# Optimization experiments

Measured on AMD Instinct MI355X. Metric: run time of the kernel, lower is better.

Reference implementation:

```python
import jax, jax.numpy as jnp
import numpy as np

B, C, H, W = 8, 128, 64, 64


def setup_inputs() -> dict:
    key = jax.random.key(0)
    ks = jax.random.split(key, 7)
    query_img = jax.random.normal(ks[0], (B, C, H, W), dtype=jnp.float32)
    key_img = jax.random.normal(ks[1], (B, C, H, W), dtype=jnp.float32)
    value_img = jax.random.normal(ks[2], (B, C, H, W), dtype=jnp.float32)
    # 1x1 conv weights == dense [out, in] matrices (kaiming-ish scale)
    scale = 1.0 / np.sqrt(C)
    Wq = jax.random.normal(ks[3], (C, C), dtype=jnp.float32) * scale
    bq = jax.random.normal(ks[4], (C,), dtype=jnp.float32) * scale
    Wk = jax.random.normal(ks[5], (C, C), dtype=jnp.float32) * scale
    bk = jax.random.normal(ks[6], (C,), dtype=jnp.float32) * scale
    return {"query_img": query_img, "key_img": key_img, "value_img": value_img,
            "Wq": Wq, "bq": bq, "Wk": Wk, "bk": bk}


def reference(query_img, key_img, value_img, Wq, bq, Wk, bk):
    b, c, h, w = query_img.shape
    hw = h * w
    # 1x1 convs as GEMMs -> token-major layout (b, hw, c_out)
    q = jnp.einsum('bchw,oc->bhwo', query_img, Wq).reshape(b, hw, -1) + bq
    k = jnp.einsum('bchw,oc->bohw', key_img, Wk).reshape(b, -1, hw) + bk[None, :, None]
    # scores scaled by sqrt(HW) (faithful: key.size(-1) == h*w in source)
    scores = jnp.einsum('bqc,bck->bqk', q, k) / jnp.sqrt(jnp.float32(hw))
    attn = jax.nn.softmax(scores, axis=-1)  # (b, hw, hw)
    v = value_img.reshape(b, c, hw).transpose(0, 2, 1)  # (b, hw, c)
    out = jnp.einsum('bqk,bkc->bqc', attn, v)  # (b, hw, c)
    out = out.transpose(0, 2, 1).reshape(b, -1, h, w)
    out = out + q.transpose(0, 2, 1).reshape(b, -1, h, w)  # residual from query proj
    return out
```

## Files before the change

### kernel.cpp

```cpp
#include <hip/hip_runtime.h>

#define BB 8
#define CC 128
#define SS 4096
#define KT 64
#define SCALE 0.015625f

typedef __attribute__((ext_vector_type(8))) short sh8;
typedef __attribute__((ext_vector_type(4))) float f32x4;

__device__ __forceinline__ float b2f(unsigned short u) {
    union { unsigned int i; float f; } x; x.i = ((unsigned int)u) << 16; return x.f;
}
__device__ __forceinline__ unsigned short f2b(float f) {
    union { float f; unsigned int i; } x; x.f = f;
    unsigned int r = x.i + 0x7fff + ((x.i >> 16) & 1);
    return (unsigned short)(r >> 16);
}
__device__ __forceinline__ unsigned short rhu(float f) {
    union { float f; unsigned int i; } x; x.f = f;
    return (unsigned short)((x.i + 0x8000) >> 16);
}

__device__ __forceinline__ void dma16(const void* g, void* l) {
    __builtin_amdgcn_global_load_lds((const __attribute__((address_space(1))) void*)g,
                                     (__attribute__((address_space(3))) void*)l,
                                     16, 0, 0);
}

__global__ __launch_bounds__(256) void cvt_kernel(
    const float* __restrict__ vimg,
    const float* __restrict__ Wq, const float* __restrict__ Wk,
    const float* __restrict__ bq, const float* __restrict__ bk,
    unsigned short* __restrict__ Vbuf,
    unsigned short* __restrict__ Wqb, unsigned short* __restrict__ Wkb,
    unsigned short* __restrict__ bqb, unsigned short* __restrict__ bkb)
{
    const int bx = blockIdx.x, tid = threadIdx.x;
    if (bx < 512) {
        const size_t base = (size_t)bx * 8192 + tid * 4;
        #pragma unroll
        for (int it = 0; it < 8; ++it) {
            const size_t i = base + (size_t)it * 1024;
            float4 v = *(const float4*)(vimg + i);
            ushort4 o;
            o.x = f2b(v.x); o.y = f2b(v.y); o.z = f2b(v.z); o.w = f2b(v.w);
            *(ushort4*)(Vbuf + i) = o;
        }
    } else {
        const int w = bx - 512;
        for (int e = w * 256 + tid; e < 33024; e += 2048) {
            float v; unsigned short* dst;
            if (e < 16384)      { v = Wq[e];         dst = Wqb + e; }
            else if (e < 32768) { v = Wk[e - 16384]; dst = Wkb + (e - 16384); }
            else if (e < 32896) { v = bq[e - 32768]; dst = bqb + (e - 32768); }
            else                { v = bk[e - 32896]; dst = bkb + (e - 32896); }
            *dst = f2b(v);
        }
    }
}

__global__ __launch_bounds__(256) void proj_kernel(
    const float* __restrict__ qimg, const float* __restrict__ kimg,
    const unsigned short* __restrict__ Wqb, const unsigned short* __restrict__ Wkb,
    const unsigned short* __restrict__ bqb, const unsigned short* __restrict__ bkb,
    unsigned short* __restrict__ Qbuf, unsigned short* __restrict__ Kbuf)
{
    __shared__ float ilds[128 * 69];

    const int z = blockIdx.z;
    const float* img = (z == 0) ? qimg : kimg;
    const unsigned short* Wb = (z == 0) ? Wqb : Wkb;
    const unsigned short* bias = (z == 0) ? bqb : bkb;
    unsigned short* outTok = (z == 0) ? Qbuf : Kbuf;

    const int tid  = threadIdx.x;
    const int wave = tid >> 6;
    const int lane = tid & 63;
    const int l15  = lane & 15;
    const int quad = lane >> 4;
    const int b     = blockIdx.y;
    const int stile = blockIdx.x;

    const float* gbase = img + (size_t)b * CC * SS + stile * 64;
    #pragma unroll
    for (int i = 0; i < 8; ++i) {
        const int l = tid + 256 * i;
        const int row = l >> 4, col = (l & 15) * 4;
        float4 v = *(const float4*)(gbase + (size_t)row * SS + col);
        float* d = ilds + row * 69 + col;
        d[0] = v.x; d[1] = v.y; d[2] = v.z; d[3] = v.w;
    }
    __syncthreads();

    const int tcol = wave * 16 + l15;
    sh8 a[4];
    #pragma unroll
    for (int kk = 0; kk < 4; ++kk)
        #pragma unroll
        for (int j = 0; j < 8; ++j)
            a[kk][j] = (short)rhu(ilds[(32 * kk + quad * 8 + j) * 69 + tcol]);

    f32x4 acc[8];
    #pragma unroll
    for (int nt = 0; nt < 8; ++nt) acc[nt] = (f32x4){0.f, 0.f, 0.f, 0.f};

    #pragma unroll
    for (int nt = 0; nt < 8; ++nt) {
        const unsigned short* wp = Wb + (size_t)(16 * nt + l15) * CC + quad * 8;
        #pragma unroll
        for (int kk = 0; kk < 4; ++kk) {
            sh8 bf = *(const sh8*)(wp + 32 * kk);
            acc[nt] = __builtin_amdgcn_mfma_f32_16x16x32_bf16(a[kk], bf, acc[nt], 0, 0, 0);
        }
    }

    #pragma unroll
    for (int nt = 0; nt < 8; ++nt) {
        const int o = 16 * nt + l15;
        const float bv = b2f(bias[o]);
        #pragma unroll
        for (int r = 0; r < 4; ++r) {
            const int s = stile * 64 + wave * 16 + quad * 4 + r;
            outTok[((size_t)b * SS + s) * CC + o] = f2b(acc[nt][r] + bv);
        }
    }
}

__global__ __launch_bounds__(256, 4) void attn_kernel(
    const unsigned short* __restrict__ Qbuf,
    const unsigned short* __restrict__ Kbuf,
    const unsigned short* __restrict__ Vbuf,
    float* __restrict__ out)
{
    __shared__ __align__(16) unsigned char smem[40960];
    unsigned char* kb = smem;
    unsigned char* vb = smem + 16384;

    const int tid  = threadIdx.x;
    const int wave = tid >> 6;
    const int lane = tid & 63;
    const int l15  = lane & 15;
    const int quad = lane >> 4;
    const int b     = blockIdx.y;
    const int qtile = blockIdx.x;
    const int qbase = qtile * 64 + wave * 16;

    unsigned char* pw = smem + 32768 + wave * 2048;

    const unsigned short* kbp = Kbuf + (size_t)b * SS * CC;
    const unsigned short* vbp = Vbuf + (size_t)b * CC * SS;

    sh8 aq[4];
    {
        const unsigned short* qp = Qbuf + ((size_t)b * SS + qbase + l15) * CC + quad * 8;
        #pragma unroll
        for (int kk = 0; kk < 4; ++kk) aq[kk] = *(const sh8*)(qp + 32 * kk);
    }

    int kGO[4], vGO[4];
    #pragma unroll
    for (int j = 0; j < 4; ++j) {
        const int krow = wave * 16 + j * 4 + (lane >> 4);
        kGO[j] = krow * 256 + (((lane & 15) ^ (krow & 7)) << 4);
        const int vrow = (wave * 4 + j) * 8 + (lane >> 3);
        vGO[j] = vrow * 8192 + (((lane & 7) ^ ((lane >> 3) & 7)) << 4);
    }

    f32x4 oacc[8];
    #pragma unroll
    for (int ct = 0; ct < 8; ++ct) oacc[ct] = (f32x4){0.f, 0.f, 0.f, 0.f};
    float lsum[4] = {0.f, 0.f, 0.f, 0.f};

    #pragma unroll
    for (int j = 0; j < 4; ++j) {
        dma16((const char*)kbp + kGO[j], kb + (wave * 4 + j) * 1024);
        dma16((const char*)vbp + vGO[j], vb + (wave * 4 + j) * 1024);
    }

    for (int it = 0; it < SS / KT; ++it) {
        __syncthreads();

        f32x4 sacc[4];
        #pragma unroll
        for (int n = 0; n < 4; ++n) {
            sacc[n] = (f32x4){0.f, 0.f, 0.f, 0.f};
            #pragma unroll
            for (int kk = 0; kk < 4; ++kk) {
                sh8 kf = *(const sh8*)(kb + (16 * n + l15) * 256
                                          + (((4 * kk + quad) ^ (l15 & 7)) << 4));
                sacc[n] = __builtin_amdgcn_mfma_f32_16x16x32_bf16(aq[kk], kf, sacc[n], 0, 0, 0);
            }
        }

        #pragma unroll
        for (int n = 0; n < 4; ++n)
            #pragma unroll
            for (int r = 0; r < 4; ++r) {
                float p = __expf(sacc[n][r] * SCALE);
                lsum[r] += p;
                const int row = quad * 4 + r, col = 16 * n + l15;
                *(unsigned short*)(pw + row * 128
                                   + (((col >> 3) ^ (row & 7)) << 4)
                                   + (col & 7) * 2) = rhu(p);
            }

        sh8 ap0 = *(const sh8*)(pw + l15 * 128 + ((quad ^ (l15 & 7)) << 4));
        #pragma unroll
        for (int ct = 0; ct < 8; ++ct) {
            sh8 bv = *(const sh8*)(vb + (16 * ct + l15) * 128
                                      + ((quad ^ (l15 & 7)) << 4));
            oacc[ct] = __builtin_amdgcn_mfma_f32_16x16x32_bf16(ap0, bv, oacc[ct], 0, 0, 0);
        }

        sh8 ap1 = *(const sh8*)(pw + l15 * 128 + (((4 + quad) ^ (l15 & 7)) << 4));
        sh8 vv[8];
        #pragma unroll
        for (int ct = 0; ct < 8; ++ct)
            vv[ct] = *(const sh8*)(vb + (16 * ct + l15) * 128
                                      + (((4 + quad) ^ (l15 & 7)) << 4));

        __syncthreads();

        if (it + 1 < SS / KT) {
            const char* gk = (const char*)kbp + (size_t)(it + 1) * KT * 256;
            const char* gv = (const char*)vbp + (size_t)(it + 1) * KT * 2;
            #pragma unroll
            for (int j = 0; j < 4; ++j) {
                dma16(gk + kGO[j], kb + (wave * 4 + j) * 1024);
                dma16(gv + vGO[j], vb + (wave * 4 + j) * 1024);
            }
        }

        #pragma unroll
        for (int ct = 0; ct < 8; ++ct)
            oacc[ct] = __builtin_amdgcn_mfma_f32_16x16x32_bf16(ap1, vv[ct], oacc[ct], 0, 0, 0);
    }

    #pragma unroll
    for (int r = 0; r < 4; ++r) {
        float v = lsum[r];
        #pragma unroll
        for (int m = 8; m >= 1; m >>= 1) v += __shfl_xor(v, m, 64);
        lsum[r] = v;
    }

    float (*oLds)[129] = (float(*)[129])smem;
    #pragma unroll
    for (int ct = 0; ct < 8; ++ct) {
        const int c = 16 * ct + l15;
        #pragma unroll
        for (int r = 0; r < 4; ++r) {
            const int qloc  = wave * 16 + quad * 4 + r;
            const int qglob = qtile * 64 + qloc;
            const float resid = b2f(Qbuf[((size_t)b * SS + qglob) * CC + c]);
            oLds[qloc][c] = oacc[ct][r] / lsum[r] + resid;
        }
    }
    __syncthreads();
    for (int idx = tid; idx < 64 * 128; idx += 256) {
        const int c = idx >> 6, q = idx & 63;
        out[((size_t)b * CC + c) * SS + qtile * 64 + q] = oLds[q][c];
    }
}

extern "C" void kernel_launch(void* const* d_in, const int* in_sizes, int n_in,
                              void* d_out, int out_size, void* d_ws, size_t ws_size,
                              hipStream_t stream) {
    const float* qimg = (const float*)d_in[0];
    const float* kimg = (const float*)d_in[1];
    const float* vimg = (const float*)d_in[2];
    const float* Wq   = (const float*)d_in[3];
    const float* bq   = (const float*)d_in[4];
    const float* Wk   = (const float*)d_in[5];
    const float* bk   = (const float*)d_in[6];
    float* out = (float*)d_out;

    unsigned short* Qbuf = (unsigned short*)d_ws;
    unsigned short* Kbuf = Qbuf + (size_t)BB * SS * CC;
    unsigned short* Vbuf = Kbuf + (size_t)BB * SS * CC;
    unsigned short* Wqb  = Vbuf + (size_t)BB * SS * CC;
    unsigned short* Wkb  = Wqb + CC * CC;
    unsigned short* bqb  = Wkb + CC * CC;
    unsigned short* bkb  = bqb + CC;

    cvt_kernel<<<dim3(520), 256, 0, stream>>>(vimg, Wq, Wk, bq, bk,
                                              Vbuf, Wqb, Wkb, bqb, bkb);
    proj_kernel<<<dim3(SS / 64, BB, 2), 256, 0, stream>>>(
        qimg, kimg, Wqb, Wkb, bqb, bkb, Qbuf, Kbuf);
    attn_kernel<<<dim3(SS / 64, BB), 256, 0, stream>>>(Qbuf, Kbuf, Vbuf, out);
}
```

Measured before the change: 224.8 us.

## Double-buffer K/V tiles and process two query sub-tiles per wave

Each wave now handles 32 query rows (two 16-row MFMA tiles), so every K/V fragment read from LDS feeds twice as many MFMAs. K/V staging becomes double-buffered, with the next tile's DMA issued right after the barrier, replacing one of the two block barriers per iteration. The grid is flattened with batch as the fastest index so neighbouring blocks share a batch's K/V in cache. The cost is 80KB of LDS and more accumulator registers, which cuts occupancy to about one block per CU and halves the grid to 256 blocks.

```diff
diff --git a/kernel.cpp b/kernel.cpp
--- a/kernel.cpp
+++ b/kernel.cpp
@@ -127,35 +127,35 @@
     }
 }
 
-__global__ __launch_bounds__(256, 4) void attn_kernel(
+__global__ __launch_bounds__(256, 1) void attn_kernel(
     const unsigned short* __restrict__ Qbuf,
     const unsigned short* __restrict__ Kbuf,
     const unsigned short* __restrict__ Vbuf,
     float* __restrict__ out)
 {
-    __shared__ __align__(16) unsigned char smem[40960];
-    unsigned char* kb = smem;
-    unsigned char* vb = smem + 16384;
+    __shared__ __align__(16) unsigned char smem[81920];
 
     const int tid  = threadIdx.x;
     const int wave = tid >> 6;
     const int lane = tid & 63;
     const int l15  = lane & 15;
     const int quad = lane >> 4;
-    const int b     = blockIdx.y;
-    const int qtile = blockIdx.x;
-    const int qbase = qtile * 64 + wave * 16;
-
-    unsigned char* pw = smem + 32768 + wave * 2048;
+    const int wgid  = blockIdx.x;
+    const int b     = wgid & 7;
+    const int qtile = wgid >> 3;
+    const int qbase = qtile * 128 + wave * 32;
+
+    unsigned char* pw = smem + 65536 + wave * 4096;
 
     const unsigned short* kbp = Kbuf + (size_t)b * SS * CC;
     const unsigned short* vbp = Vbuf + (size_t)b * CC * SS;
 
-    sh8 aq[4];
-    {
-        const unsigned short* qp = Qbuf + ((size_t)b * SS + qbase + l15) * CC + quad * 8;
-        #pragma unroll
-        for (int kk = 0; kk < 4; ++kk) aq[kk] = *(const sh8*)(qp + 32 * kk);
+    sh8 aq[2][4];
+    #pragma unroll
+    for (int m = 0; m < 2; ++m) {
+        const unsigned short* qp = Qbuf + ((size_t)b * SS + qbase + m * 16 + l15) * CC + quad * 8;
+        #pragma unroll
+        for (int kk = 0; kk < 4; ++kk) aq[m][kk] = *(const sh8*)(qp + 32 * kk);
     }
 
     int kGO[4], vGO[4];
@@ -167,100 +167,114 @@
         vGO[j] = vrow * 8192 + (((lane & 7) ^ ((lane >> 3) & 7)) << 4);
     }
 
-    f32x4 oacc[8];
-    #pragma unroll
-    for (int ct = 0; ct < 8; ++ct) oacc[ct] = (f32x4){0.f, 0.f, 0.f, 0.f};
-    float lsum[4] = {0.f, 0.f, 0.f, 0.f};
+    f32x4 oacc[2][8];
+    #pragma unroll
+    for (int m = 0; m < 2; ++m)
+        #pragma unroll
+        for (int ct = 0; ct < 8; ++ct) oacc[m][ct] = (f32x4){0.f, 0.f, 0.f, 0.f};
+    float lsum[2][4] = {{0.f, 0.f, 0.f, 0.f}, {0.f, 0.f, 0.f, 0.f}};
 
     #pragma unroll
     for (int j = 0; j < 4; ++j) {
-        dma16((const char*)kbp + kGO[j], kb + (wave * 4 + j) * 1024);
-        dma16((const char*)vbp + vGO[j], vb + (wave * 4 + j) * 1024);
+        dma16((const char*)kbp + kGO[j], smem + (wave * 4 + j) * 1024);
+        dma16((const char*)vbp + vGO[j], smem + 32768 + (wave * 4 + j) * 1024);
     }
 
     for (int it = 0; it < SS / KT; ++it) {
-        __syncthreads();
-
-        f32x4 sacc[4];
+        unsigned char* kb = smem + ((it & 1) << 14);
+        unsigned char* vb = smem + 32768 + ((it & 1) << 14);
+
+        asm volatile("s_waitcnt vmcnt(0)" ::: "memory");
+        __builtin_amdgcn_s_barrier();
+
+        if (it + 1 < SS / KT) {
+            unsigned char* kbn = smem + (((it + 1) & 1) << 14);
+            unsigned char* vbn = smem + 32768 + (((it + 1) & 1) << 14);
+            const char* gk = (const char*)kbp + (size_t)(it + 1) * KT * 256;
+            const char* gv = (const char*)vbp + (size_t)(it + 1) * KT * 2;
+            #pragma unroll
+            for (int j = 0; j < 4; ++j) {
+                dma16(gk + kGO[j], kbn + (wave * 4 + j) * 1024);
+                dma16(gv + vGO[j], vbn + (wave * 4 + j) * 1024);
+            }
+        }
+
+        f32x4 sacc[2][4];
+        #pragma unroll
+        for (int m = 0; m < 2; ++m)
+            #pragma unroll
+            for (int n = 0; n < 4; ++n) sacc[m][n] = (f32x4){0.f, 0.f, 0.f, 0.f};
         #pragma unroll
         for (int n = 0; n < 4; ++n) {
-            sacc[n] = (f32x4){0.f, 0.f, 0.f, 0.f};
             #pragma unroll
             for (int kk = 0; kk < 4; ++kk) {
                 sh8 kf = *(const sh8*)(kb + (16 * n + l15) * 256
                                           + (((4 * kk + quad) ^ (l15 & 7)) << 4));
-                sacc[n] = __builtin_amdgcn_mfma_f32_16x16x32_bf16(aq[kk], kf, sacc[n], 0, 0, 0);
+                sacc[0][n] = __builtin_amdgcn_mfma_f32_16x16x32_bf16(aq[0][kk], kf, sacc[0][n], 0, 0, 0);
+                sacc[1][n] = __builtin_amdgcn_mfma_f32_16x16x32_bf16(aq[1][kk], kf, sacc[1][n], 0, 0, 0);
             }
         }
 
         #pragma unroll
-        for (int n = 0; n < 4; ++n)
+        for (int m = 0; m < 2; ++m)
+            #pragma unroll
+            for (int n = 0; n < 4; ++n)
+                #pragma unroll
+                for (int r = 0; r < 4; ++r) {
+                    float p = __expf(sacc[m][n][r] * SCALE);
+                    lsum[m][r] += p;
+                    const int row = m * 16 + quad * 4 + r, col = 16 * n + l15;
+                    *(unsigned short*)(pw + row * 128
+                                       + (((col >> 3) ^ (row & 7)) << 4)
+                                       + (col & 7) * 2) = rhu(p);
+                }
+
+        #pragma unroll
+        for (int ks = 0; ks < 2; ++ks) {
+            sh8 ap0 = *(const sh8*)(pw + l15 * 128
+                                       + (((ks * 4 + quad) ^ (l15 & 7)) << 4));
+            sh8 ap1 = *(const sh8*)(pw + (16 + l15) * 128
+                                       + (((ks * 4 + quad) ^ (l15 & 7)) << 4));
+            #pragma unroll
+            for (int ct = 0; ct < 8; ++ct) {
+                sh8 bv = *(const sh8*)(vb + (16 * ct + l15) * 128
+                                          + (((ks * 4 + quad) ^ (l15 & 7)) << 4));
+                oacc[0][ct] = __builtin_amdgcn_mfma_f32_16x16x32_bf16(ap0, bv, oacc[0][ct], 0, 0, 0);
+                oacc[1][ct] = __builtin_amdgcn_mfma_f32_16x16x32_bf16(ap1, bv, oacc[1][ct], 0, 0, 0);
+            }
+        }
+    }
+
+    #pragma unroll
+    for (int m = 0; m < 2; ++m)
+        #pragma unroll
+        for (int r = 0; r < 4; ++r) {
+            float v = lsum[m][r];
+            #pragma unroll
+            for (int s = 8; s >= 1; s >>= 1) v += __shfl_xor(v, s, 64);
+            lsum[m][r] = v;
+        }
+
+    __syncthreads();
+
+    float (*oLds)[129] = (float(*)[129])smem;
+    #pragma unroll
+    for (int m = 0; m < 2; ++m)
+        #pragma unroll
+        for (int ct = 0; ct < 8; ++ct) {
+            const int c = 16 * ct + l15;
             #pragma unroll
             for (int r = 0; r < 4; ++r) {
-                float p = __expf(sacc[n][r] * SCALE);
-                lsum[r] += p;
-                const int row = quad * 4 + r, col = 16 * n + l15;
-                *(unsigned short*)(pw + row * 128
-                                   + (((col >> 3) ^ (row & 7)) << 4)
-                                   + (col & 7) * 2) = rhu(p);
+                const int qloc  = wave * 32 + m * 16 + quad * 4 + r;
+                const int qglob = qtile * 128 + qloc;
+                const float resid = b2f(Qbuf[((size_t)b * SS + qglob) * CC + c]);
+                oLds[qloc][c] = oacc[m][ct][r] / lsum[m][r] + resid;
             }
-
-        sh8 ap0 = *(const sh8*)(pw + l15 * 128 + ((quad ^ (l15 & 7)) << 4));
-        #pragma unroll
-        for (int ct = 0; ct < 8; ++ct) {
-            sh8 bv = *(const sh8*)(vb + (16 * ct + l15) * 128
-                                      + ((quad ^ (l15 & 7)) << 4));
-            oacc[ct] = __builtin_amdgcn_mfma_f32_16x16x32_bf16(ap0, bv, oacc[ct], 0, 0, 0);
-        }
-
-        sh8 ap1 = *(const sh8*)(pw + l15 * 128 + (((4 + quad) ^ (l15 & 7)) << 4));
-        sh8 vv[8];
-        #pragma unroll
-        for (int ct = 0; ct < 8; ++ct)
-            vv[ct] = *(const sh8*)(vb + (16 * ct + l15) * 128
-                                      + (((4 + quad) ^ (l15 & 7)) << 4));
-
-        __syncthreads();
-
-        if (it + 1 < SS / KT) {
-            const char* gk = (const char*)kbp + (size_t)(it + 1) * KT * 256;
-            const char* gv = (const char*)vbp + (size_t)(it + 1) * KT * 2;
-            #pragma unroll
-            for (int j = 0; j < 4; ++j) {
-                dma16(gk + kGO[j], kb + (wave * 4 + j) * 1024);
-                dma16(gv + vGO[j], vb + (wave * 4 + j) * 1024);
-            }
-        }
-
-        #pragma unroll
-        for (int ct = 0; ct < 8; ++ct)
-            oacc[ct] = __builtin_amdgcn_mfma_f32_16x16x32_bf16(ap1, vv[ct], oacc[ct], 0, 0, 0);
-    }
-
-    #pragma unroll
-    for (int r = 0; r < 4; ++r) {
-        float v = lsum[r];
-        #pragma unroll
-        for (int m = 8; m >= 1; m >>= 1) v += __shfl_xor(v, m, 64);
-        lsum[r] = v;
-    }
-
-    float (*oLds)[129] = (float(*)[129])smem;
-    #pragma unroll
-    for (int ct = 0; ct < 8; ++ct) {
-        const int c = 16 * ct + l15;
-        #pragma unroll
-        for (int r = 0; r < 4; ++r) {
-            const int qloc  = wave * 16 + quad * 4 + r;
-            const int qglob = qtile * 64 + qloc;
-            const float resid = b2f(Qbuf[((size_t)b * SS + qglob) * CC + c]);
-            oLds[qloc][c] = oacc[ct][r] / lsum[r] + resid;
-        }
-    }
+        }
     __syncthreads();
-    for (int idx = tid; idx < 64 * 128; idx += 256) {
-        const int c = idx >> 6, q = idx & 63;
-        out[((size_t)b * CC + c) * SS + qtile * 64 + q] = oLds[q][c];
+    for (int idx = tid; idx < 128 * 128; idx += 256) {
+        const int c = idx >> 7, q = idx & 127;
+        out[((size_t)b * CC + c) * SS + qtile * 128 + q] = oLds[q][c];
     }
 }
 
@@ -288,5 +302,5 @@
                                               Vbuf, Wqb, Wkb, bqb, bkb);
     proj_kernel<<<dim3(SS / 64, BB, 2), 256, 0, stream>>>(
         qimg, kimg, Wqb, Wkb, bqb, bkb, Qbuf, Kbuf);
-    attn_kernel<<<dim3(SS / 64, BB), 256, 0, stream>>>(Qbuf, Kbuf, Vbuf, out);
-}
+    attn_kernel<<<dim3(BB * (SS / 128)), 256, 0, stream>>>(Qbuf, Kbuf, Vbuf, out);
+}
```

New measurement: 248.8 us. 10.7% more time.
